# Kernel optimization log

Hardware: AMD Instinct MI355X
Metric: run time of the kernel (lower is better)

Reference implementation:

```python
import jax, jax.numpy as jnp
import numpy as np

N_NODES = 50000
N_RAND_EDGES = 800000
LEAKY_SLOPE = 0.2


def gat_layer(x, edge_index, W, a_src, a_dst, b, num_heads):
    """Multi-head GAT layer. W: [Din, Dout]; heads split Dout; concat output."""
    N = x.shape[0]
    Dout = W.shape[1]
    Dh = Dout // num_heads
    z = (x @ W).reshape(N, num_heads, Dh)                      # [N,H,Dh]
    src = edge_index[0]
    dst = edge_index[1]
    alpha_src = jnp.einsum('nhd,hd->nh', z, a_src)             # [N,H]
    alpha_dst = jnp.einsum('nhd,hd->nh', z, a_dst)             # [N,H]
    e = jax.nn.leaky_relu(alpha_src[src] + alpha_dst[dst], LEAKY_SLOPE)  # [E,H]
    # segment softmax over incoming edges of each dst node
    m = jax.ops.segment_max(e, dst, num_segments=N)            # [N,H]
    e = jnp.exp(e - m[dst])
    denom = jax.ops.segment_sum(e, dst, num_segments=N)        # [N,H]
    alpha = e / (denom[dst] + 1e-16)                           # [E,H]
    msg = z[src] * alpha[:, :, None]                           # [E,H,Dh]
    out = jax.ops.segment_sum(msg, dst, num_segments=N)        # [N,H,Dh]
    return out.reshape(N, Dout) + b


def setup_inputs() -> dict:
    key = jax.random.key(0)
    ks = jax.random.split(key, 12)
    input_dim, hidden_dim, num_classes, num_heads = 128, 64, 16, 8
    x = jax.random.normal(ks[0], (N_NODES, input_dim), dtype=jnp.float32)
    rand_edges = jax.random.randint(ks[1], (2, N_RAND_EDGES), 0, N_NODES, dtype=jnp.int32)
    self_loops = jnp.tile(jnp.arange(N_NODES, dtype=jnp.int32), (2, 1))
    edge_indices = jnp.concatenate([rand_edges, self_loops], axis=1)   # [2, 850000]

    def glorot(k, shape):
        fan = sum(shape[-2:]) if len(shape) > 1 else shape[0]
        return jax.random.normal(k, shape, dtype=jnp.float32) * (2.0 / fan) ** 0.5

    W1 = glorot(ks[2], (input_dim, hidden_dim))
    a_src1 = glorot(ks[3], (num_heads, hidden_dim // num_heads))
    a_dst1 = glorot(ks[4], (num_heads, hidden_dim // num_heads))
    b1 = jnp.zeros((hidden_dim,), dtype=jnp.float32)
    W2 = glorot(ks[5], (hidden_dim, num_classes))
    a_src2 = glorot(ks[6], (1, num_classes))
    a_dst2 = glorot(ks[7], (1, num_classes))
    b2 = jnp.zeros((num_classes,), dtype=jnp.float32)
    return {"x": x, "edge_indices": edge_indices,
            "W1": W1, "a_src1": a_src1, "a_dst1": a_dst1, "b1": b1,
            "W2": W2, "a_src2": a_src2, "a_dst2": a_dst2, "b2": b2}


def reference(x, edge_indices, W1, a_src1, a_dst1, b1, W2, a_src2, a_dst2, b2):
    # Dropout is identity in eval mode.
    h = gat_layer(x, edge_indices, W1, a_src1, a_dst1, b1, num_heads=8)
    h = jax.nn.elu(h)
    return gat_layer(h, edge_indices, W2, a_src2, a_dst2, b2, num_heads=1)
```

## Files before the change

kernel.cpp:

```cpp
#include <hip/hip_runtime.h>
#include <hip/hip_fp16.h>


#define LRELU(v) ((v) > 0.f ? (v) : 0.2f * (v))

__global__ void kA(const float* __restrict__ x, const float* __restrict__ W1,
                   const float* __restrict__ a_src1, const float* __restrict__ a_dst1,
                   const int* __restrict__ src, const int* __restrict__ dst,
                   int* __restrict__ deg, unsigned short* __restrict__ csr,
                   __half* __restrict__ z1h, __half* __restrict__ as1h,
                   float* __restrict__ ad1, int N, int E) {
    __shared__ float xs[64][132];
    __shared__ float wt[64][132];
    __shared__ float avs[128];
    int b = blockIdx.x;
    int tid = threadIdx.x;
    bool is_gemm = (b < 1564) && ((b & 1) == 0);

    if (!is_gemm) {
        int rank = (b < 1564) ? (b >> 1) : (b - 782);
        for (int e = rank * 256 + tid; e < E; e += 1024 * 256) {
            int d = dst[e];
            int pos = atomicAdd(&deg[d], 1);
            if (pos < 64) csr[(d << 6) + pos] = (unsigned short)src[e];
        }
        return;
    }

    int n0 = (b >> 1) * 64;
    for (int idx = tid; idx < 8192; idx += 256) {
        int k = idx >> 6, c = idx & 63;
        wt[c][k] = W1[idx];
    }
    for (int idx = tid; idx < 2048; idx += 256) {
        int r = idx >> 5, q = idx & 31;
        int n = n0 + r; if (n >= N) n = N - 1;
        float4 v = ((const float4*)(x + (size_t)n * 128))[q];
        *(float4*)&xs[r][q * 4] = v;
    }
    if (tid < 128) avs[tid] = (tid < 64) ? a_src1[tid] : a_dst1[tid - 64];
    __syncthreads();

    int rg = tid >> 4, cg2 = tid & 15;
    float acc[4][4] = {};
    for (int k4 = 0; k4 < 32; ++k4) {
        float4 xv[4], wv[4];
#pragma unroll
        for (int i = 0; i < 4; ++i) xv[i] = *(const float4*)&xs[rg * 4 + i][k4 * 4];
#pragma unroll
        for (int j = 0; j < 4; ++j) wv[j] = *(const float4*)&wt[cg2 * 4 + j][k4 * 4];
#pragma unroll
        for (int i = 0; i < 4; ++i)
#pragma unroll
            for (int j = 0; j < 4; ++j) {
                acc[i][j] += xv[i].x * wv[j].x;
                acc[i][j] += xv[i].y * wv[j].y;
                acc[i][j] += xv[i].z * wv[j].z;
                acc[i][j] += xv[i].w * wv[j].w;
            }
    }
    int h = cg2 >> 1, db = (cg2 & 1) * 4;
    float pas[4], pad_[4];
#pragma unroll
    for (int i = 0; i < 4; ++i) {
        float s = 0.f, dd = 0.f;
#pragma unroll
        for (int j = 0; j < 4; ++j) {
            s  += acc[i][j] * avs[h * 8 + db + j];
            dd += acc[i][j] * avs[64 + h * 8 + db + j];
        }
        pas[i] = s; pad_[i] = dd;
    }
#pragma unroll
    for (int i = 0; i < 4; ++i) {
        pas[i]  += __shfl_xor(pas[i], 1, 64);
        pad_[i] += __shfl_xor(pad_[i], 1, 64);
    }
#pragma unroll
    for (int i = 0; i < 4; ++i) {
        int n = n0 + rg * 4 + i;
        if (n < N) {
            union { __half2 h2[2]; uint2 u; } pk;
            pk.h2[0] = __floats2half2_rn(acc[i][0], acc[i][1]);
            pk.h2[1] = __floats2half2_rn(acc[i][2], acc[i][3]);
            *(uint2*)&z1h[(size_t)n * 64 + cg2 * 4] = pk.u;
            if ((cg2 & 1) == 0) {
                as1h[(size_t)n * 8 + h] = __float2half_rn(pas[i]);
                ad1[(size_t)n * 8 + h] = pad_[i];
            }
        }
    }
}

__global__ void kg1(const int* __restrict__ deg, const unsigned short* __restrict__ csr,
                    const __half* __restrict__ as1h, const float* __restrict__ ad1,
                    const __half* __restrict__ z1h, const float* __restrict__ b1,
                    const float* __restrict__ W2, const float* __restrict__ a_src2,
                    const float* __restrict__ a_dst2,
                    __half* __restrict__ z2h, float* __restrict__ as2,
                    float* __restrict__ ad2, int N) {
    __shared__ int s_idx[4][64];
    __shared__ float asv[4][64][8];
    __shared__ float hs[4][64];
    int lane = threadIdx.x & 63, wid = threadIdx.x >> 6;
    int d = blockIdx.x * 4 + wid;
    if (d >= N) return;
    int q = lane & 7, g = lane >> 3;
    int cnt = min(deg[d], 64);
    float adv = ad1[(size_t)d * 8 + q];
    if (lane < cnt) {
        int s = csr[(d << 6) + lane];
        s_idx[wid][lane] = s;
        uint4 raw = *(const uint4*)(as1h + (size_t)s * 8);
        const __half2* ap = (const __half2*)&raw;
        float2 u0 = __half22float2(ap[0]), u1 = __half22float2(ap[1]);
        float2 u2 = __half22float2(ap[2]), u3 = __half22float2(ap[3]);
        *(float4*)&asv[wid][lane][0] = make_float4(u0.x, u0.y, u1.x, u1.y);
        *(float4*)&asv[wid][lane][4] = make_float4(u2.x, u2.y, u3.x, u3.y);
    }
    float a0 = 0.f, a1 = 0.f, a2 = 0.f, a3 = 0.f;
    float a4 = 0.f, a5 = 0.f, a6 = 0.f, a7 = 0.f, dsum = 0.f;
#pragma unroll 2
    for (int j = g; j < cnt; j += 8) {
        int s = s_idx[wid][j];
        float ev = asv[wid][j][q] + adv;
        float w = __expf(LRELU(ev));
        float4 raw = *(const float4*)(z1h + (size_t)s * 64 + q * 8);
        const __half2* hp = (const __half2*)&raw;
        float2 f0 = __half22float2(hp[0]), f1 = __half22float2(hp[1]);
        float2 f2 = __half22float2(hp[2]), f3 = __half22float2(hp[3]);
        a0 += w * f0.x; a1 += w * f0.y; a2 += w * f1.x; a3 += w * f1.y;
        a4 += w * f2.x; a5 += w * f2.y; a6 += w * f3.x; a7 += w * f3.y;
        dsum += w;
    }
#pragma unroll
    for (int m = 8; m <= 32; m <<= 1) {
        a0 += __shfl_xor(a0, m, 64); a1 += __shfl_xor(a1, m, 64);
        a2 += __shfl_xor(a2, m, 64); a3 += __shfl_xor(a3, m, 64);
        a4 += __shfl_xor(a4, m, 64); a5 += __shfl_xor(a5, m, 64);
        a6 += __shfl_xor(a6, m, 64); a7 += __shfl_xor(a7, m, 64);
        dsum += __shfl_xor(dsum, m, 64);
    }
    float inv = 1.f / dsum;
    float hv[8] = {a0 * inv + b1[q * 8 + 0], a1 * inv + b1[q * 8 + 1],
                   a2 * inv + b1[q * 8 + 2], a3 * inv + b1[q * 8 + 3],
                   a4 * inv + b1[q * 8 + 4], a5 * inv + b1[q * 8 + 5],
                   a6 * inv + b1[q * 8 + 6], a7 * inv + b1[q * 8 + 7]};
#pragma unroll
    for (int i = 0; i < 8; ++i) hv[i] = hv[i] > 0.f ? hv[i] : expm1f(hv[i]);
    if (g == 0) {
        *(float4*)&hs[wid][q * 8]     = make_float4(hv[0], hv[1], hv[2], hv[3]);
        *(float4*)&hs[wid][q * 8 + 4] = make_float4(hv[4], hv[5], hv[6], hv[7]);
    }
    int kq = lane >> 4, c = lane & 15;
    float zc = 0.f;
#pragma unroll
    for (int k = 0; k < 16; ++k)
        zc += hs[wid][kq * 16 + k] * W2[(kq * 16 + k) * 16 + c];
    zc += __shfl_xor(zc, 16, 64);
    zc += __shfl_xor(zc, 32, 64);
    float ps = zc * a_src2[c];
    float pd = zc * a_dst2[c];
#pragma unroll
    for (int m = 1; m < 16; m <<= 1) {
        ps += __shfl_xor(ps, m, 64);
        pd += __shfl_xor(pd, m, 64);
    }
    if (lane < 16) z2h[(size_t)d * 16 + lane] = __float2half_rn(zc);
    if (lane == 0) { as2[d] = ps; ad2[d] = pd; }
}

__global__ void kg2(const int* __restrict__ deg, const unsigned short* __restrict__ csr,
                    const float* __restrict__ as2, const float* __restrict__ ad2,
                    const __half* __restrict__ z2h, const float* __restrict__ b2,
                    float* __restrict__ out, int N) {
    __shared__ int s_idx[4][64];
    __shared__ float asv[4][64];
    int lane = threadIdx.x & 63, wid = threadIdx.x >> 6;
    int d = blockIdx.x * 4 + wid;
    if (d >= N) return;
    int q = lane & 3, g = lane >> 2;
    int cnt = min(deg[d], 64);
    float adv = ad2[d];
    if (lane < cnt) {
        int s = csr[(d << 6) + lane];
        s_idx[wid][lane] = s;
        asv[wid][lane] = as2[s];
    }
    float ax = 0.f, ay = 0.f, az = 0.f, aw = 0.f, dsum = 0.f;
#pragma unroll 2
    for (int j = g; j < cnt; j += 16) {
        int s = s_idx[wid][j];
        float ev = asv[wid][j] + adv;
        float w = __expf(LRELU(ev));
        uint2 raw = *(const uint2*)(z2h + (size_t)s * 16 + q * 4);
        const __half2* hp = (const __half2*)&raw;
        float2 f0 = __half22float2(hp[0]), f1 = __half22float2(hp[1]);
        ax += w * f0.x; ay += w * f0.y; az += w * f1.x; aw += w * f1.y;
        dsum += w;
    }
#pragma unroll
    for (int m = 4; m <= 32; m <<= 1) {
        ax += __shfl_xor(ax, m, 64); ay += __shfl_xor(ay, m, 64);
        az += __shfl_xor(az, m, 64); aw += __shfl_xor(aw, m, 64);
        dsum += __shfl_xor(dsum, m, 64);
    }
    if (g == 0) {
        float inv = 1.f / dsum;
        float4 o = make_float4(ax * inv + b2[q * 4], ay * inv + b2[q * 4 + 1],
                               az * inv + b2[q * 4 + 2], aw * inv + b2[q * 4 + 3]);
        *(float4*)&out[(size_t)d * 16 + q * 4] = o;
    }
}

extern "C" void kernel_launch(void* const* d_in, const int* in_sizes, int n_in,
                              void* d_out, int out_size, void* d_ws, size_t ws_size,
                              hipStream_t stream) {
    const float* x      = (const float*)d_in[0];
    const int*   ei     = (const int*)d_in[1];
    const float* W1     = (const float*)d_in[2];
    const float* a_src1 = (const float*)d_in[3];
    const float* a_dst1 = (const float*)d_in[4];
    const float* b1     = (const float*)d_in[5];
    const float* W2     = (const float*)d_in[6];
    const float* a_src2 = (const float*)d_in[7];
    const float* a_dst2 = (const float*)d_in[8];
    const float* b2     = (const float*)d_in[9];
    float* out = (float*)d_out;

    const int N = in_sizes[0] / 128;
    const int E = in_sizes[1] / 2;
    const int* src = ei;
    const int* dst = ei + E;

    float* ws = (float*)d_ws;
    size_t off = 0;
    __half* z1h = (__half*)(ws + off); off += (size_t)N * 32;
    __half* as1h = (__half*)(ws + off); off += (size_t)N * 4;
    float* ad1 = ws + off; off += (size_t)N * 8;
    __half* z2h = (__half*)(ws + off); off += (size_t)N * 8;
    float* as2 = ws + off; off += (size_t)N;
    float* ad2 = ws + off; off += (size_t)N;
    unsigned short* csr = (unsigned short*)(ws + off); off += (size_t)N * 32;
    int* deg = (int*)(ws + off); off += (size_t)N;

    hipMemsetAsync(deg, 0, (size_t)N * sizeof(int), stream);

    kA<<<1806, 256, 0, stream>>>(x, W1, a_src1, a_dst1, src, dst, deg, csr,
                                 z1h, as1h, ad1, N, E);
    kg1<<<(N + 3) / 4, 256, 0, stream>>>(deg, csr, as1h, ad1, z1h, b1, W2,
                                         a_src2, a_dst2, z2h, as2, ad2, N);
    kg2<<<(N + 3) / 4, 256, 0, stream>>>(deg, csr, as2, ad2, z2h, b2, out, N);
}
```

Baseline: 187.6 us.

## Make GAT aggregation kernels persistent with double-buffered neighbor prefetch

Both aggregation kernels become grid-stride persistent loops over destination nodes, launched with a fixed 2048 blocks. While the current node is aggregated, the next node's neighbor indices and source attention scores are prefetched into a second shared-memory buffer. The goal is to hide the latency of the index and score gathers behind the feature gather and compute. In exchange, the lane<cnt guard is dropped, so every lane loads a CSR slot and gathers a score even when the node has few neighbors. This adds memory traffic and can read uninitialized indices. The fixed grid may also lower occupancy.

New measurement: 192.6 us. 1.03x slower.

```diff
diff --git a/kernel.cpp b/kernel.cpp
--- a/kernel.cpp
+++ b/kernel.cpp
@@ -99,117 +99,160 @@
                     const float* __restrict__ a_dst2,
                     __half* __restrict__ z2h, float* __restrict__ as2,
                     float* __restrict__ ad2, int N) {
-    __shared__ int s_idx[4][64];
-    __shared__ float asv[4][64][8];
+    __shared__ int s_idx[2][4][64];
+    __shared__ float asv[2][4][64][8];
     __shared__ float hs[4][64];
     int lane = threadIdx.x & 63, wid = threadIdx.x >> 6;
-    int d = blockIdx.x * 4 + wid;
-    if (d >= N) return;
+    int d0 = blockIdx.x * 4 + wid;
+    if (d0 >= N) return;
     int q = lane & 7, g = lane >> 3;
-    int cnt = min(deg[d], 64);
-    float adv = ad1[(size_t)d * 8 + q];
-    if (lane < cnt) {
-        int s = csr[(d << 6) + lane];
-        s_idx[wid][lane] = s;
+    int kq = lane >> 4, c = lane & 15;
+    int stride = gridDim.x * 4;
+    int cnt[2];
+    float adv[2];
+
+    {
+        cnt[0] = min(deg[d0], 64);
+        adv[0] = ad1[(size_t)d0 * 8 + q];
+        int s = csr[(d0 << 6) + lane];
+        s_idx[0][wid][lane] = s;
         uint4 raw = *(const uint4*)(as1h + (size_t)s * 8);
         const __half2* ap = (const __half2*)&raw;
         float2 u0 = __half22float2(ap[0]), u1 = __half22float2(ap[1]);
         float2 u2 = __half22float2(ap[2]), u3 = __half22float2(ap[3]);
-        *(float4*)&asv[wid][lane][0] = make_float4(u0.x, u0.y, u1.x, u1.y);
-        *(float4*)&asv[wid][lane][4] = make_float4(u2.x, u2.y, u3.x, u3.y);
-    }
-    float a0 = 0.f, a1 = 0.f, a2 = 0.f, a3 = 0.f;
-    float a4 = 0.f, a5 = 0.f, a6 = 0.f, a7 = 0.f, dsum = 0.f;
+        *(float4*)&asv[0][wid][lane][0] = make_float4(u0.x, u0.y, u1.x, u1.y);
+        *(float4*)&asv[0][wid][lane][4] = make_float4(u2.x, u2.y, u3.x, u3.y);
+    }
+
+    int buf = 0;
+    for (int d = d0; d < N; d += stride, buf ^= 1) {
+        int dn = d + stride;
+        if (dn < N) {
+            cnt[buf ^ 1] = min(deg[dn], 64);
+            adv[buf ^ 1] = ad1[(size_t)dn * 8 + q];
+            int s = csr[(dn << 6) + lane];
+            s_idx[buf ^ 1][wid][lane] = s;
+            uint4 raw = *(const uint4*)(as1h + (size_t)s * 8);
+            const __half2* ap = (const __half2*)&raw;
+            float2 u0 = __half22float2(ap[0]), u1 = __half22float2(ap[1]);
+            float2 u2 = __half22float2(ap[2]), u3 = __half22float2(ap[3]);
+            *(float4*)&asv[buf ^ 1][wid][lane][0] = make_float4(u0.x, u0.y, u1.x, u1.y);
+            *(float4*)&asv[buf ^ 1][wid][lane][4] = make_float4(u2.x, u2.y, u3.x, u3.y);
+        }
+
+        int cn = cnt[buf];
+        float advc = adv[buf];
+        float a0 = 0.f, a1 = 0.f, a2 = 0.f, a3 = 0.f;
+        float a4 = 0.f, a5 = 0.f, a6 = 0.f, a7 = 0.f, dsum = 0.f;
 #pragma unroll 2
-    for (int j = g; j < cnt; j += 8) {
-        int s = s_idx[wid][j];
-        float ev = asv[wid][j][q] + adv;
-        float w = __expf(LRELU(ev));
-        float4 raw = *(const float4*)(z1h + (size_t)s * 64 + q * 8);
-        const __half2* hp = (const __half2*)&raw;
-        float2 f0 = __half22float2(hp[0]), f1 = __half22float2(hp[1]);
-        float2 f2 = __half22float2(hp[2]), f3 = __half22float2(hp[3]);
-        a0 += w * f0.x; a1 += w * f0.y; a2 += w * f1.x; a3 += w * f1.y;
-        a4 += w * f2.x; a5 += w * f2.y; a6 += w * f3.x; a7 += w * f3.y;
-        dsum += w;
-    }
-#pragma unroll
-    for (int m = 8; m <= 32; m <<= 1) {
-        a0 += __shfl_xor(a0, m, 64); a1 += __shfl_xor(a1, m, 64);
-        a2 += __shfl_xor(a2, m, 64); a3 += __shfl_xor(a3, m, 64);
-        a4 += __shfl_xor(a4, m, 64); a5 += __shfl_xor(a5, m, 64);
-        a6 += __shfl_xor(a6, m, 64); a7 += __shfl_xor(a7, m, 64);
-        dsum += __shfl_xor(dsum, m, 64);
-    }
-    float inv = 1.f / dsum;
-    float hv[8] = {a0 * inv + b1[q * 8 + 0], a1 * inv + b1[q * 8 + 1],
-                   a2 * inv + b1[q * 8 + 2], a3 * inv + b1[q * 8 + 3],
-                   a4 * inv + b1[q * 8 + 4], a5 * inv + b1[q * 8 + 5],
-                   a6 * inv + b1[q * 8 + 6], a7 * inv + b1[q * 8 + 7]};
-#pragma unroll
-    for (int i = 0; i < 8; ++i) hv[i] = hv[i] > 0.f ? hv[i] : expm1f(hv[i]);
-    if (g == 0) {
-        *(float4*)&hs[wid][q * 8]     = make_float4(hv[0], hv[1], hv[2], hv[3]);
-        *(float4*)&hs[wid][q * 8 + 4] = make_float4(hv[4], hv[5], hv[6], hv[7]);
-    }
-    int kq = lane >> 4, c = lane & 15;
-    float zc = 0.f;
-#pragma unroll
-    for (int k = 0; k < 16; ++k)
-        zc += hs[wid][kq * 16 + k] * W2[(kq * 16 + k) * 16 + c];
-    zc += __shfl_xor(zc, 16, 64);
-    zc += __shfl_xor(zc, 32, 64);
-    float ps = zc * a_src2[c];
-    float pd = zc * a_dst2[c];
-#pragma unroll
-    for (int m = 1; m < 16; m <<= 1) {
-        ps += __shfl_xor(ps, m, 64);
-        pd += __shfl_xor(pd, m, 64);
-    }
-    if (lane < 16) z2h[(size_t)d * 16 + lane] = __float2half_rn(zc);
-    if (lane == 0) { as2[d] = ps; ad2[d] = pd; }
+        for (int j = g; j < cn; j += 8) {
+            int s = s_idx[buf][wid][j];
+            float ev = asv[buf][wid][j][q] + advc;
+            float w = __expf(LRELU(ev));
+            float4 raw = *(const float4*)(z1h + (size_t)s * 64 + q * 8);
+            const __half2* hp = (const __half2*)&raw;
+            float2 f0 = __half22float2(hp[0]), f1 = __half22float2(hp[1]);
+            float2 f2 = __half22float2(hp[2]), f3 = __half22float2(hp[3]);
+            a0 += w * f0.x; a1 += w * f0.y; a2 += w * f1.x; a3 += w * f1.y;
+            a4 += w * f2.x; a5 += w * f2.y; a6 += w * f3.x; a7 += w * f3.y;
+            dsum += w;
+        }
+#pragma unroll
+        for (int m = 8; m <= 32; m <<= 1) {
+            a0 += __shfl_xor(a0, m, 64); a1 += __shfl_xor(a1, m, 64);
+            a2 += __shfl_xor(a2, m, 64); a3 += __shfl_xor(a3, m, 64);
+            a4 += __shfl_xor(a4, m, 64); a5 += __shfl_xor(a5, m, 64);
+            a6 += __shfl_xor(a6, m, 64); a7 += __shfl_xor(a7, m, 64);
+            dsum += __shfl_xor(dsum, m, 64);
+        }
+        float inv = 1.f / dsum;
+        float hv[8] = {a0 * inv + b1[q * 8 + 0], a1 * inv + b1[q * 8 + 1],
+                       a2 * inv + b1[q * 8 + 2], a3 * inv + b1[q * 8 + 3],
+                       a4 * inv + b1[q * 8 + 4], a5 * inv + b1[q * 8 + 5],
+                       a6 * inv + b1[q * 8 + 6], a7 * inv + b1[q * 8 + 7]};
+#pragma unroll
+        for (int i = 0; i < 8; ++i) hv[i] = hv[i] > 0.f ? hv[i] : expm1f(hv[i]);
+        if (g == 0) {
+            *(float4*)&hs[wid][q * 8]     = make_float4(hv[0], hv[1], hv[2], hv[3]);
+            *(float4*)&hs[wid][q * 8 + 4] = make_float4(hv[4], hv[5], hv[6], hv[7]);
+        }
+        float zc = 0.f;
+#pragma unroll
+        for (int k = 0; k < 16; ++k)
+            zc += hs[wid][kq * 16 + k] * W2[(kq * 16 + k) * 16 + c];
+        zc += __shfl_xor(zc, 16, 64);
+        zc += __shfl_xor(zc, 32, 64);
+        float ps = zc * a_src2[c];
+        float pd = zc * a_dst2[c];
+#pragma unroll
+        for (int m = 1; m < 16; m <<= 1) {
+            ps += __shfl_xor(ps, m, 64);
+            pd += __shfl_xor(pd, m, 64);
+        }
+        if (lane < 16) z2h[(size_t)d * 16 + lane] = __float2half_rn(zc);
+        if (lane == 0) { as2[d] = ps; ad2[d] = pd; }
+    }
 }
 
 __global__ void kg2(const int* __restrict__ deg, const unsigned short* __restrict__ csr,
                     const float* __restrict__ as2, const float* __restrict__ ad2,
                     const __half* __restrict__ z2h, const float* __restrict__ b2,
                     float* __restrict__ out, int N) {
-    __shared__ int s_idx[4][64];
-    __shared__ float asv[4][64];
+    __shared__ int s_idx[2][4][64];
+    __shared__ float asv[2][4][64];
     int lane = threadIdx.x & 63, wid = threadIdx.x >> 6;
-    int d = blockIdx.x * 4 + wid;
-    if (d >= N) return;
+    int d0 = blockIdx.x * 4 + wid;
+    if (d0 >= N) return;
     int q = lane & 3, g = lane >> 2;
-    int cnt = min(deg[d], 64);
-    float adv = ad2[d];
-    if (lane < cnt) {
-        int s = csr[(d << 6) + lane];
-        s_idx[wid][lane] = s;
-        asv[wid][lane] = as2[s];
-    }
-    float ax = 0.f, ay = 0.f, az = 0.f, aw = 0.f, dsum = 0.f;
+    int stride = gridDim.x * 4;
+    int cnt[2];
+    float adv[2];
+
+    {
+        cnt[0] = min(deg[d0], 64);
+        adv[0] = ad2[d0];
+        int s = csr[(d0 << 6) + lane];
+        s_idx[0][wid][lane] = s;
+        asv[0][wid][lane] = as2[s];
+    }
+
+    int buf = 0;
+    for (int d = d0; d < N; d += stride, buf ^= 1) {
+        int dn = d + stride;
+        if (dn < N) {
+            cnt[buf ^ 1] = min(deg[dn], 64);
+            adv[buf ^ 1] = ad2[dn];
+            int s = csr[(dn << 6) + lane];
+            s_idx[buf ^ 1][wid][lane] = s;
+            asv[buf ^ 1][wid][lane] = as2[s];
+        }
+
+        int cn = cnt[buf];
+        float advc = adv[buf];
+        float ax = 0.f, ay = 0.f, az = 0.f, aw = 0.f, dsum = 0.f;
 #pragma unroll 2
-    for (int j = g; j < cnt; j += 16) {
-        int s = s_idx[wid][j];
-        float ev = asv[wid][j] + adv;
-        float w = __expf(LRELU(ev));
-        uint2 raw = *(const uint2*)(z2h + (size_t)s * 16 + q * 4);
-        const __half2* hp = (const __half2*)&raw;
-        float2 f0 = __half22float2(hp[0]), f1 = __half22float2(hp[1]);
-        ax += w * f0.x; ay += w * f0.y; az += w * f1.x; aw += w * f1.y;
-        dsum += w;
-    }
-#pragma unroll
-    for (int m = 4; m <= 32; m <<= 1) {
-        ax += __shfl_xor(ax, m, 64); ay += __shfl_xor(ay, m, 64);
-        az += __shfl_xor(az, m, 64); aw += __shfl_xor(aw, m, 64);
-        dsum += __shfl_xor(dsum, m, 64);
-    }
-    if (g == 0) {
-        float inv = 1.f / dsum;
-        float4 o = make_float4(ax * inv + b2[q * 4], ay * inv + b2[q * 4 + 1],
-                               az * inv + b2[q * 4 + 2], aw * inv + b2[q * 4 + 3]);
-        *(float4*)&out[(size_t)d * 16 + q * 4] = o;
+        for (int j = g; j < cn; j += 16) {
+            int s = s_idx[buf][wid][j];
+            float ev = asv[buf][wid][j] + advc;
+            float w = __expf(LRELU(ev));
+            uint2 raw = *(const uint2*)(z2h + (size_t)s * 16 + q * 4);
+            const __half2* hp = (const __half2*)&raw;
+            float2 f0 = __half22float2(hp[0]), f1 = __half22float2(hp[1]);
+            ax += w * f0.x; ay += w * f0.y; az += w * f1.x; aw += w * f1.y;
+            dsum += w;
+        }
+#pragma unroll
+        for (int m = 4; m <= 32; m <<= 1) {
+            ax += __shfl_xor(ax, m, 64); ay += __shfl_xor(ay, m, 64);
+            az += __shfl_xor(az, m, 64); aw += __shfl_xor(aw, m, 64);
+            dsum += __shfl_xor(dsum, m, 64);
+        }
+        if (g == 0) {
+            float inv = 1.f / dsum;
+            float4 o = make_float4(ax * inv + b2[q * 4], ay * inv + b2[q * 4 + 1],
+                                   az * inv + b2[q * 4 + 2], aw * inv + b2[q * 4 + 3]);
+            *(float4*)&out[(size_t)d * 16 + q * 4] = o;
+        }
     }
 }
 
@@ -248,7 +291,7 @@
 
     kA<<<1806, 256, 0, stream>>>(x, W1, a_src1, a_dst1, src, dst, deg, csr,
                                  z1h, as1h, ad1, N, E);
-    kg1<<<(N + 3) / 4, 256, 0, stream>>>(deg, csr, as1h, ad1, z1h, b1, W2,
-                                         a_src2, a_dst2, z2h, as2, ad2, N);
-    kg2<<<(N + 3) / 4, 256, 0, stream>>>(deg, csr, as2, ad2, z2h, b2, out, N);
-}
+    kg1<<<2048, 256, 0, stream>>>(deg, csr, as1h, ad1, z1h, b1, W2,
+                                  a_src2, a_dst2, z2h, as2, ad2, N);
+    kg2<<<2048, 256, 0, stream>>>(deg, csr, as2, ad2, z2h, b2, out, N);
+}
```
